# Kernel tuning notes

Hardware: AMD Instinct MI355X
Metric: run time of the kernel (lower is better)

## Reference

```python
import jax, jax.numpy as jnp
import numpy as np

S, P, H, E = 32, 32, 128, 64        # scenes, peds/scene, h_dim, embedding_dim
B1, B2 = 512, 1024                  # mlp_pre_pool hidden, bottleneck_dim
M1 = 1024                           # decoder mlp hidden
N = S * P
T = 12                              # seq_len (decode horizon)
BN_INV = 1.0 / np.sqrt(1.0 + 1e-5)  # eval-mode BatchNorm, running mean=0 var=1


def setup_inputs() -> dict:
    key = jax.random.key(0)
    ks = jax.random.split(key, 32)
    rn = lambda k, sh, s=0.05: jax.random.normal(k, sh, dtype=jnp.float32) * s
    inp = {
        'last_pos': rn(ks[0], (N, 2), 1.0),
        'last_pos_rel': rn(ks[1], (N, 2), 1.0),
        'h0': rn(ks[2], (N, H), 0.1),
        'c0': rn(ks[3], (N, H), 0.1),
        'seq_start_end': jnp.stack([jnp.arange(S) * P, (jnp.arange(S) + 1) * P], 1).astype(jnp.int32),
        # decoder spatial embedding Linear(2, E)
        'emb_W': rn(ks[4], (E, 2)), 'emb_b': rn(ks[5], (E,)),
        # LSTM (torch gate order i,f,g,o)
        'lstm_Wih': rn(ks[6], (4 * H, E)), 'lstm_Whh': rn(ks[7], (4 * H, H)),
        'lstm_bih': rn(ks[8], (4 * H,)), 'lstm_bhh': rn(ks[9], (4 * H,)),
        # hidden2pos Linear(H, 2)
        'pos_W': rn(ks[10], (2, H)), 'pos_b': rn(ks[11], (2,)),
        # pool_net spatial embedding Linear(2, E)
        'sp_W': rn(ks[12], (E, 2)), 'sp_b': rn(ks[13], (E,)),
        # mlp_pre_pool: Linear(E+H, 512)+BN+ReLU, Linear(512, 1024)+BN+ReLU
        'pp1_W': rn(ks[14], (B1, E + H)), 'pp1_b': rn(ks[15], (B1,)),
        'pp1_g': 1.0 + rn(ks[16], (B1,)), 'pp1_be': rn(ks[17], (B1,)),
        'pp2_W': rn(ks[18], (B2, B1)), 'pp2_b': rn(ks[19], (B2,)),
        'pp2_g': 1.0 + rn(ks[20], (B2,)), 'pp2_be': rn(ks[21], (B2,)),
        # decoder mlp: Linear(H+1024, 1024)+BN+ReLU, Linear(1024, H)+BN+ReLU
        'm1_W': rn(ks[22], (M1, H + B2)), 'm1_b': rn(ks[23], (M1,)),
        'm1_g': 1.0 + rn(ks[24], (M1,)), 'm1_be': rn(ks[25], (M1,)),
        'm2_W': rn(ks[26], (H, M1)), 'm2_b': rn(ks[27], (H,)),
        'm2_g': 1.0 + rn(ks[28], (H,)), 'm2_be': rn(ks[29], (H,)),
    }
    return inp


def _bn(x, g, b):
    return x * BN_INV * g + b


def reference(last_pos, last_pos_rel, h0, c0, seq_start_end,
              emb_W, emb_b, lstm_Wih, lstm_Whh, lstm_bih, lstm_bhh,
              pos_W, pos_b, sp_W, sp_b,
              pp1_W, pp1_b, pp1_g, pp1_be, pp2_W, pp2_b, pp2_g, pp2_be,
              m1_W, m1_b, m1_g, m1_be, m2_W, m2_b, m2_g, m2_be):
    # seq_start_end encodes uniform scenes of size P; pooling is done per scene.
    def step(carry, _):
        h, c, lp, din = carry  # h,c:[N,H]  lp:[N,2]  din:[N,E]
        gates = din @ lstm_Wih.T + lstm_bih + h @ lstm_Whh.T + lstm_bhh
        i, f, g_, o = jnp.split(gates, 4, axis=-1)
        c2 = jax.nn.sigmoid(f) * c + jax.nn.sigmoid(i) * jnp.tanh(g_)
        h2 = jax.nn.sigmoid(o) * jnp.tanh(c2)
        rel_pos = h2 @ pos_W.T + pos_b          # [N,2]
        curr = rel_pos + lp                     # [N,2]
        # ---- PoolHiddenNet: per-scene all-pairs gather -> MLP -> max ----
        ps = curr.reshape(S, P, 2)
        rel = ps[:, None, :, :] - ps[:, :, None, :]   # [s,i,j] = pos_j - pos_i
        rel = rel / jnp.maximum(jnp.linalg.norm(rel, axis=-1, keepdims=True), 1e-12)
        emb = rel @ sp_W.T + sp_b                      # [S,P,P,E]
        hj = jnp.broadcast_to(h2.reshape(S, 1, P, H), (S, P, P, H))
        x = jnp.concatenate([emb, hj], -1)             # [S,P,P,E+H]
        x = jax.nn.relu(_bn(x @ pp1_W.T + pp1_b, pp1_g, pp1_be))
        x = jax.nn.relu(_bn(x @ pp2_W.T + pp2_b, pp2_g, pp2_be))
        pool = x.max(axis=2).reshape(N, B2)            # max over neighbours j
        # ---- hidden refinement MLP ----
        dh = jnp.concatenate([h2, pool], 1)
        dh = jax.nn.relu(_bn(dh @ m1_W.T + m1_b, m1_g, m1_be))
        dh = jax.nn.relu(_bn(dh @ m2_W.T + m2_b, m2_g, m2_be))
        din2 = rel_pos @ emb_W.T + emb_b
        return (dh, c2, curr, din2), rel_pos

    din0 = last_pos_rel @ emb_W.T + emb_b
    _, preds = jax.lax.scan(step, (h0, c0, last_pos, din0), None, length=T)
    return preds  # [T, N, 2] predicted relative displacements
```

## Files before the change

### kernel.cpp

```cpp
#include <hip/hip_runtime.h>
#include <hip/hip_bf16.h>
#include <math.h>

#define DEVFN __device__ __forceinline__

constexpr float BN_INV = 0.99999500003749971f;

DEVFN float sigm(float x) { return 1.0f / (1.0f + expf(-x)); }

DEVFN unsigned short f2bf(float f) {
    __hip_bfloat16 b = __float2bfloat16(f);
    return *reinterpret_cast<unsigned short*>(&b);
}
DEVFN float bf2f(unsigned short u) {
    unsigned int x = ((unsigned int)u) << 16;
    return *reinterpret_cast<float*>(&x);
}
DEVFN void splitf(float v, unsigned short& h, unsigned short& l) {
    h = f2bf(v);
    l = f2bf(v - bf2f(h));
}
DEVFN unsigned int pack2(unsigned short a, unsigned short b) {
    return (unsigned int)a | ((unsigned int)b << 16);
}

typedef __attribute__((ext_vector_type(8))) short short8;
typedef __attribute__((ext_vector_type(4))) float f32x4;

#define ASYNC_COPY16(gsrc, ldst)                                                            \
    __builtin_amdgcn_global_load_lds((const __attribute__((address_space(1))) unsigned int*)(gsrc), \
                                     (__attribute__((address_space(3))) unsigned int*)(ldst), 16, 0, 0)


__global__ void pre_misc(
    const float* __restrict__ Wih, const float* __restrict__ Whh,
    const float* __restrict__ bih, const float* __restrict__ bhh,
    float* __restrict__ WgT, float* __restrict__ bg,
    const float* __restrict__ pp1W, const float* __restrict__ pp1g,
    float* __restrict__ Wh1T,
    const float* __restrict__ spW, const float* __restrict__ spb,
    const float* __restrict__ pp1b, const float* __restrict__ pp1be,
    float* __restrict__ Mp, float* __restrict__ c1,
    const float* __restrict__ lp, const float* __restrict__ lpr,
    const float* __restrict__ h0, const float* __restrict__ c0,
    const float* __restrict__ embW, const float* __restrict__ embb,
    float* __restrict__ h_st, float* __restrict__ c_st,
    float* __restrict__ curr, float* __restrict__ din) {
    int bid = blockIdx.x, t = threadIdx.x;
    if (bid < 384) {
        int idx = bid * 256 + t;
        int k = idx >> 9, tt = idx & 511;
        WgT[idx] = (k < 64) ? Wih[tt * 64 + k] : Whh[tt * 128 + (k - 64)];
        if (idx < 512) bg[idx] = bih[idx] + bhh[idx];
    } else if (bid < 640) {
        int idx = (bid - 384) * 256 + t;
        int h = idx >> 9, k = idx & 511;
        Wh1T[idx] = pp1W[k * 192 + 64 + h] * (BN_INV * pp1g[k]);
    } else if (bid < 642) {
        int k = (bid - 640) * 256 + t;
        float m0 = 0.f, m1 = 0.f, c0v = 0.f;
        for (int e = 0; e < 64; e++) {
            float w = pp1W[k * 192 + e];
            m0 += spW[e * 2] * w; m1 += spW[e * 2 + 1] * w; c0v += spb[e] * w;
        }
        float s = BN_INV * pp1g[k];
        Mp[k] = m0 * s; Mp[512 + k] = m1 * s;
        c1[k] = (c0v + pp1b[k]) * s + pp1be[k];
    } else {
        int idx = (bid - 642) * 256 + t;
        h_st[idx] = h0[idx];
        c_st[idx] = c0[idx];
        if (idx < 1024 * 2) curr[idx] = lp[idx];
        if (idx < 1024 * 64) {
            int n = idx >> 6, e = idx & 63;
            din[idx] = fmaf(lpr[n * 2], embW[e * 2], fmaf(lpr[n * 2 + 1], embW[e * 2 + 1], embb[e]));
        }
    }
}

__global__ void pre_w2bf(const float* __restrict__ W, const float* __restrict__ b,
                         const float* __restrict__ g, const float* __restrict__ be,
                         unsigned short* __restrict__ Wbf, float* __restrict__ cv, int swz) {
    int idx = blockIdx.x * blockDim.x + threadIdx.x;
    int ko = idx >> 9, k = idx & 511;
    float s = BN_INV * g[ko];
    int outk = swz ? ((k & ~63) | ((((k >> 3) & 7) ^ (ko & 7)) << 3) | (k & 7)) : k;
    Wbf[(ko << 9) + outk] = f2bf(W[idx] * s);
    if (idx < 1024) cv[idx] = b[idx] * s + be[idx];
}

__global__ void pre_w1split(const float* __restrict__ W, const float* __restrict__ b,
                            const float* __restrict__ g, const float* __restrict__ be,
                            unsigned short* __restrict__ Wh, unsigned short* __restrict__ Wl,
                            float* __restrict__ cv) {
    int idx = blockIdx.x * blockDim.x + threadIdx.x;
    int ko = idx / 1152;
    float s = BN_INV * g[ko];
    unsigned short h, l;
    splitf(W[idx] * s, h, l);
    Wh[idx] = h; Wl[idx] = l;
    if (idx < 1024) {
        float s2 = BN_INV * g[idx];
        cv[idx] = b[idx] * s2 + be[idx];
    }
}

__global__ void pre_w2split(const float* __restrict__ W, const float* __restrict__ b,
                            const float* __restrict__ g, const float* __restrict__ be,
                            unsigned short* __restrict__ Wh, unsigned short* __restrict__ Wl,
                            float* __restrict__ cv) {
    int idx = blockIdx.x * blockDim.x + threadIdx.x;
    int ko = idx >> 10;
    float s = BN_INV * g[ko];
    unsigned short h, l;
    splitf(W[idx] * s, h, l);
    Wh[idx] = h; Wl[idx] = l;
    if (idx < 128) {
        float s2 = BN_INV * g[idx];
        cv[idx] = b[idx] * s2 + be[idx];
    }
}


__global__ __launch_bounds__(512) void k_lstm(
    const float* __restrict__ WgT, const float* __restrict__ bg,
    float* __restrict__ h_st, float* __restrict__ c_st,
    float* __restrict__ din, float* __restrict__ curr,
    unsigned short* __restrict__ h2h, unsigned short* __restrict__ h2l,
    const float* __restrict__ posW, const float* __restrict__ posb,
    const float* __restrict__ embW, const float* __restrict__ embb,
    const float* __restrict__ Wh1T, const float* __restrict__ c1,
    float* __restrict__ Hp, int doHp,
    float* __restrict__ preds) {
    int n0 = blockIdx.x << 2;
    int t = threadIdx.x;
    __shared__ float xs[4][256];
    __shared__ float gates[4][512];
    __shared__ float h2s[4][128];
    __shared__ float rp[4][2];
#pragma unroll
    for (int u = 0; u < 2; u++) {
        int lin = t + (u << 9);
        int r = lin >> 8, k = lin & 255;
        float v = 0.f;
        if (k < 64) v = din[(n0 + r) * 64 + k];
        else if (k < 192) v = h_st[(n0 + r) * 128 + (k - 64)];
        xs[r][k] = v;
    }
    __syncthreads();
    float a0 = bg[t], a1 = a0, a2 = a0, a3 = a0;
#pragma unroll 4
    for (int k = 0; k < 192; k++) {
        float w = WgT[(k << 9) + t];
        a0 = fmaf(xs[0][k], w, a0);
        a1 = fmaf(xs[1][k], w, a1);
        a2 = fmaf(xs[2][k], w, a2);
        a3 = fmaf(xs[3][k], w, a3);
    }
    gates[0][t] = a0; gates[1][t] = a1; gates[2][t] = a2; gates[3][t] = a3;
    __syncthreads();
    {
        int r = t >> 7, hx = t & 127;
        float ig = sigm(gates[r][hx]);
        float fg = sigm(gates[r][128 + hx]);
        float gg = tanhf(gates[r][256 + hx]);
        float og = sigm(gates[r][384 + hx]);
        float c2 = fmaf(fg, c_st[(n0 + r) * 128 + hx], ig * gg);
        float h2 = og * tanhf(c2);
        c_st[(n0 + r) * 128 + hx] = c2;
        unsigned short sh, sl;
        splitf(h2, sh, sl);
        h2h[(n0 + r) * 128 + hx] = sh;
        h2l[(n0 + r) * 128 + hx] = sl;
        h2s[r][hx] = h2;
    }
    __syncthreads();
    int wv = t >> 6, l = t & 63;
    if (wv < 4) {
        float p0 = fmaf(h2s[wv][l], posW[l], h2s[wv][l + 64] * posW[l + 64]);
        float p1 = fmaf(h2s[wv][l], posW[128 + l], h2s[wv][l + 64] * posW[192 + l]);
#pragma unroll
        for (int off = 32; off > 0; off >>= 1) {
            p0 += __shfl_down(p0, off, 64);
            p1 += __shfl_down(p1, off, 64);
        }
        if (l == 0) { rp[wv][0] = p0 + posb[0]; rp[wv][1] = p1 + posb[1]; }
    }
    __syncthreads();
    if (t < 256) {
        int r = t >> 6, e = t & 63;
        float r0 = rp[r][0], r1 = rp[r][1];
        din[(n0 + r) * 64 + e] = fmaf(r0, embW[e * 2], fmaf(r1, embW[e * 2 + 1], embb[e]));
        if (e == 0) {
            preds[(n0 + r) * 2] = r0; preds[(n0 + r) * 2 + 1] = r1;
            curr[(n0 + r) * 2] += r0; curr[(n0 + r) * 2 + 1] += r1;
        }
    }
    if (doHp) {
        float cc = c1[t];
        float q0 = cc, q1 = cc, q2 = cc, q3 = cc;
#pragma unroll 4
        for (int h = 0; h < 128; h++) {
            float w = Wh1T[(h << 9) + t];
            q0 = fmaf(h2s[0][h], w, q0);
            q1 = fmaf(h2s[1][h], w, q1);
            q2 = fmaf(h2s[2][h], w, q2);
            q3 = fmaf(h2s[3][h], w, q3);
        }
        Hp[((n0 + 0) << 9) + t] = q0;
        Hp[((n0 + 1) << 9) + t] = q1;
        Hp[((n0 + 2) << 9) + t] = q2;
        Hp[((n0 + 3) << 9) + t] = q3;
    }
}

__global__ __launch_bounds__(256) void k_x1(
    const float* __restrict__ Hp, const float* __restrict__ Mp,
    const float* __restrict__ curr, unsigned short* __restrict__ x1g) {
    int bid = blockIdx.x;
    int c = bid & 7, q = bid >> 3;
    int i = q & 31, g = q >> 5;
    int s = (g << 3) + c;
    int si = (s << 5) + i;
    int t = threadIdx.x;
    __shared__ float rx[32], ry[32];
    __shared__ float m0s[512], m1s[512];
    for (int u = t; u < 512; u += 256) { m0s[u] = Mp[u]; m1s[u] = Mp[512 + u]; }
    if (t < 32) {
        int jg = (s << 5) + t;
        float dx = curr[jg * 2] - curr[si * 2];
        float dy = curr[jg * 2 + 1] - curr[si * 2 + 1];
        float den = fmaxf(sqrtf(dx * dx + dy * dy), 1e-12f);
        rx[t] = dx / den; ry[t] = dy / den;
    }
    __syncthreads();
    int j = t >> 3, c8 = t & 7;
    float rxv = rx[j], ryv = ry[j];
    const float* hp = Hp + (((s << 5) + j) << 9);
    unsigned short* op = x1g + ((size_t)((si << 5) + j) << 9);
    int swz = (c8 ^ (j & 7)) << 3;
#pragma unroll
    for (int kt = 0; kt < 512; kt += 64) {
        int k = kt + (c8 << 3);
        float4 ha = *(const float4*)(hp + k);
        float4 hb = *(const float4*)(hp + k + 4);
        uint4 o;
        o.x = pack2(f2bf(fmaxf(fmaf(rxv, m0s[k + 0], fmaf(ryv, m1s[k + 0], ha.x)), 0.f)),
                    f2bf(fmaxf(fmaf(rxv, m0s[k + 1], fmaf(ryv, m1s[k + 1], ha.y)), 0.f)));
        o.y = pack2(f2bf(fmaxf(fmaf(rxv, m0s[k + 2], fmaf(ryv, m1s[k + 2], ha.z)), 0.f)),
                    f2bf(fmaxf(fmaf(rxv, m0s[k + 3], fmaf(ryv, m1s[k + 3], ha.w)), 0.f)));
        o.z = pack2(f2bf(fmaxf(fmaf(rxv, m0s[k + 4], fmaf(ryv, m1s[k + 4], hb.x)), 0.f)),
                    f2bf(fmaxf(fmaf(rxv, m0s[k + 5], fmaf(ryv, m1s[k + 5], hb.y)), 0.f)));
        o.w = pack2(f2bf(fmaxf(fmaf(rxv, m0s[k + 6], fmaf(ryv, m1s[k + 6], hb.z)), 0.f)),
                    f2bf(fmaxf(fmaf(rxv, m0s[k + 7], fmaf(ryv, m1s[k + 7], hb.w)), 0.f)));
        *(uint4*)(op + kt + swz) = o;
    }
}

__global__ __launch_bounds__(1024, 4) void k_pool_g(
    const unsigned short* __restrict__ x1g, const unsigned short* __restrict__ W2bf,
    const float* __restrict__ c2v,
    unsigned short* __restrict__ poolh, unsigned short* __restrict__ pooll) {
    int bid = blockIdx.x;
    int c = bid & 7, q = bid >> 3;
    int inner = q & 15, g = q >> 4;
    int s = (g << 3) + c;
    int rb = inner >> 2;
    int koB = (inner & 3) << 8;
    int t = threadIdx.x;
    int lane = t & 63, wv = t >> 6;
    int quad = lane >> 4, l15 = lane & 15;
    int wr = wv >> 2, wc = wv & 3;
    int qrow = wr << 6, qcol = wc << 6;
    __shared__ unsigned short As[2][256 * 64];
    __shared__ unsigned short Bs[2][256 * 64];
    f32x4 acc[4][4];
#pragma unroll
    for (int a = 0; a < 4; a++)
#pragma unroll
        for (int b = 0; b < 4; b++) acc[a][b] = (f32x4){0.f, 0.f, 0.f, 0.f};

    int rlane = lane >> 3;
    int clane = (lane & 7) << 3;
    const unsigned short* gA = x1g + (size_t)((s << 10) + (rb << 8) + (wv << 4) + rlane) * 512 + clane;
    const unsigned short* gB = W2bf + (size_t)(koB + (wv << 4) + rlane) * 512 + clane;
    const unsigned short* pa0 = &As[0][((qrow + l15) << 6) + ((quad ^ (l15 & 7)) << 3)];
    const unsigned short* pb0 = &Bs[0][((qcol + l15) << 6) + ((quad ^ (l15 & 7)) << 3)];
    const unsigned short* pa1 = &As[0][((qrow + l15) << 6) + (((4 + quad) ^ (l15 & 7)) << 3)];
    const unsigned short* pb1 = &Bs[0][((qcol + l15) << 6) + (((4 + quad) ^ (l15 & 7)) << 3)];

#define POOL_STAGE(kt, buf)                                           \
    do {                                                              \
        unsigned short* lA = &As[buf][wv << 10];                      \
        unsigned short* lB = &Bs[buf][wv << 10];                      \
        ASYNC_COPY16(gA + (kt), lA);                                  \
        ASYNC_COPY16(gA + (kt) + 8 * 512, lA + (8 << 6));             \
        ASYNC_COPY16(gB + (kt), lB);                                  \
        ASYNC_COPY16(gB + (kt) + 8 * 512, lB + (8 << 6));             \
    } while (0)

    POOL_STAGE(0, 0);
    __syncthreads();
    for (int i = 0; i < 8; i++) {
        if (i < 7) POOL_STAGE((i + 1) << 6, (i + 1) & 1);
        int off = (i & 1) << 14;
        short8 aF[4], bF[4];
#pragma unroll
        for (int a = 0; a < 4; a++) aF[a] = *(const short8*)(pa0 + off + (a << 10));
#pragma unroll
        for (int b = 0; b < 4; b++) bF[b] = *(const short8*)(pb0 + off + (b << 10));
#pragma unroll
        for (int a = 0; a < 4; a++)
#pragma unroll
            for (int b = 0; b < 4; b++)
                acc[a][b] = __builtin_amdgcn_mfma_f32_16x16x32_bf16(aF[a], bF[b], acc[a][b], 0, 0, 0);
#pragma unroll
        for (int a = 0; a < 4; a++) aF[a] = *(const short8*)(pa1 + off + (a << 10));
#pragma unroll
        for (int b = 0; b < 4; b++) bF[b] = *(const short8*)(pb1 + off + (b << 10));
#pragma unroll
        for (int a = 0; a < 4; a++)
#pragma unroll
            for (int b = 0; b < 4; b++)
                acc[a][b] = __builtin_amdgcn_mfma_f32_16x16x32_bf16(aF[a], bF[b], acc[a][b], 0, 0, 0);
        __syncthreads();
    }
#undef POOL_STAGE

    float mx0[4], mx1[4];
#pragma unroll
    for (int b = 0; b < 4; b++) {
        float m = acc[0][b].x;
#pragma unroll
        for (int a = 0; a < 2; a++) {
            m = fmaxf(m, acc[a][b].x); m = fmaxf(m, acc[a][b].y);
            m = fmaxf(m, acc[a][b].z); m = fmaxf(m, acc[a][b].w);
        }
        m = fmaxf(m, __shfl_xor(m, 16));
        m = fmaxf(m, __shfl_xor(m, 32));
        mx0[b] = m;
        float n = acc[2][b].x;
#pragma unroll
        for (int a = 2; a < 4; a++) {
            n = fmaxf(n, acc[a][b].x); n = fmaxf(n, acc[a][b].y);
            n = fmaxf(n, acc[a][b].z); n = fmaxf(n, acc[a][b].w);
        }
        n = fmaxf(n, __shfl_xor(n, 16));
        n = fmaxf(n, __shfl_xor(n, 32));
        mx1[b] = n;
    }
    float v0 = (quad == 0) ? mx0[0] : (quad == 1) ? mx0[1] : (quad == 2) ? mx0[2] : mx0[3];
    float v1 = (quad == 0) ? mx1[0] : (quad == 1) ? mx1[1] : (quad == 2) ? mx1[2] : mx1[3];
    int col = koB + qcol + (quad << 4) + l15;
    int i0 = (rb << 3) + (wr << 1);
    int si0 = (s << 5) + i0;
    float bias = c2v[col];
    float w0 = fmaxf(v0 + bias, 0.f);
    float w1 = fmaxf(v1 + bias, 0.f);
    unsigned short h0, l0, h1, l1;
    splitf(w0, h0, l0); splitf(w1, h1, l1);
    poolh[si0 * 1024 + col] = h0; pooll[si0 * 1024 + col] = l0;
    poolh[(si0 + 1) * 1024 + col] = h1; pooll[(si0 + 1) * 1024 + col] = l1;
}

__global__ __launch_bounds__(256) void k_pool_mfma(
    const float* __restrict__ Hp, const float* __restrict__ Mp,
    const unsigned short* __restrict__ W2bf,
    const float* __restrict__ c2v, const float* __restrict__ curr,
    unsigned short* __restrict__ poolh, unsigned short* __restrict__ pooll) {
    int s = blockIdx.z;
    int rb = blockIdx.y;
    int koBase = blockIdx.x << 7;
    int t = threadIdx.x;
    int lane = t & 63, wv = t >> 6;
    int quad = lane >> 4, l15 = lane & 15;
    int qrow = (wv >> 1) << 6;
    int qcol = (wv & 1) << 6;

    __shared__ unsigned short As[128 * 40];
    __shared__ unsigned short Bs[128 * 40];
    __shared__ float rx[128], ry[128];

    if (t < 128) {
        int iL = t >> 5, j = t & 31;
        int ig = (s << 5) + (rb << 2) + iL;
        int jg = (s << 5) + j;
        float dx = curr[jg * 2] - curr[ig * 2];
        float dy = curr[jg * 2 + 1] - curr[ig * 2 + 1];
        float den = fmaxf(sqrtf(dx * dx + dy * dy), 1e-12f);
        rx[t] = dx / den; ry[t] = dy / den;
    }
    __syncthreads();

    f32x4 acc[4][4];
#pragma unroll
    for (int a = 0; a < 4; a++)
#pragma unroll
        for (int b = 0; b < 4; b++) acc[a][b] = (f32x4){0.f, 0.f, 0.f, 0.f};

    int r0 = t >> 3, c4 = (t & 7) << 2;
    int bn = t >> 1, bk = (t & 1) << 4;

    for (int kt = 0; kt < 512; kt += 32) {
#pragma unroll
        for (int p = 0; p < 4; p++) {
            int rr = r0 + (p << 5);
            int j = rr & 31;
            int kg = kt + c4;
            float4 hv = *(const float4*)(Hp + (((s << 5) + j) << 9) + kg);
            float4 m0 = *(const float4*)(Mp + kg);
            float4 m1 = *(const float4*)(Mp + 512 + kg);
            float rxv = rx[rr], ryv = ry[rr];
            float v0 = fmaxf(fmaf(rxv, m0.x, fmaf(ryv, m1.x, hv.x)), 0.f);
            float v1 = fmaxf(fmaf(rxv, m0.y, fmaf(ryv, m1.y, hv.y)), 0.f);
            float v2 = fmaxf(fmaf(rxv, m0.z, fmaf(ryv, m1.z, hv.z)), 0.f);
            float v3 = fmaxf(fmaf(rxv, m0.w, fmaf(ryv, m1.w, hv.w)), 0.f);
            unsigned int u0 = pack2(f2bf(v0), f2bf(v1));
            unsigned int u1 = pack2(f2bf(v2), f2bf(v3));
            *(uint2*)(&As[rr * 40 + c4]) = make_uint2(u0, u1);
        }
        {
            const unsigned short* src = W2bf + (((koBase + bn) << 9) + kt + bk);
            uint4 w0 = *(const uint4*)src;
            uint4 w1 = *(const uint4*)(src + 8);
            *(uint4*)(&Bs[bn * 40 + bk]) = w0;
            *(uint4*)(&Bs[bn * 40 + bk + 8]) = w1;
        }
        __syncthreads();
        short8 bF[4];
#pragma unroll
        for (int b = 0; b < 4; b++)
            bF[b] = *(const short8*)(&Bs[(qcol + (b << 4) + l15) * 40 + (quad << 3)]);
#pragma unroll
        for (int a = 0; a < 4; a++) {
            short8 aF = *(const short8*)(&As[(qrow + (a << 4) + l15) * 40 + (quad << 3)]);
#pragma unroll
            for (int b = 0; b < 4; b++)
                acc[a][b] = __builtin_amdgcn_mfma_f32_16x16x32_bf16(aF, bF[b], acc[a][b], 0, 0, 0);
        }
        __syncthreads();
    }

    float mx0[4], mx1[4];
#pragma unroll
    for (int b = 0; b < 4; b++) {
        float m = acc[0][b].x;
#pragma unroll
        for (int a = 0; a < 2; a++) {
            m = fmaxf(m, acc[a][b].x); m = fmaxf(m, acc[a][b].y);
            m = fmaxf(m, acc[a][b].z); m = fmaxf(m, acc[a][b].w);
        }
        m = fmaxf(m, __shfl_xor(m, 16));
        m = fmaxf(m, __shfl_xor(m, 32));
        mx0[b] = m;
        float n = acc[2][b].x;
#pragma unroll
        for (int a = 2; a < 4; a++) {
            n = fmaxf(n, acc[a][b].x); n = fmaxf(n, acc[a][b].y);
            n = fmaxf(n, acc[a][b].z); n = fmaxf(n, acc[a][b].w);
        }
        n = fmaxf(n, __shfl_xor(n, 16));
        n = fmaxf(n, __shfl_xor(n, 32));
        mx1[b] = n;
    }
    float v0 = (quad == 0) ? mx0[0] : (quad == 1) ? mx0[1] : (quad == 2) ? mx0[2] : mx0[3];
    float v1 = (quad == 0) ? mx1[0] : (quad == 1) ? mx1[1] : (quad == 2) ? mx1[2] : mx1[3];
    int col = koBase + qcol + (quad << 4) + l15;
    int i0 = (rb << 2) + ((wv >> 1) << 1);
    int si0 = (s << 5) + i0;
    float bias = c2v[col];
    float w0 = fmaxf(v0 + bias, 0.f);
    float w1 = fmaxf(v1 + bias, 0.f);
    unsigned short h0, l0, h1, l1;
    splitf(w0, h0, l0); splitf(w1, h1, l1);
    poolh[si0 * 1024 + col] = h0; pooll[si0 * 1024 + col] = l0;
    poolh[(si0 + 1) * 1024 + col] = h1; pooll[(si0 + 1) * 1024 + col] = l1;
}

__global__ __launch_bounds__(256) void k_m1_mfma(
    const unsigned short* __restrict__ h2h, const unsigned short* __restrict__ h2l,
    const unsigned short* __restrict__ poolh, const unsigned short* __restrict__ pooll,
    const unsigned short* __restrict__ M1h, const unsigned short* __restrict__ M1l,
    const float* __restrict__ cm1,
    unsigned short* __restrict__ dh1h, unsigned short* __restrict__ dh1l) {
    int rowBase = blockIdx.y << 6;
    int koBase = blockIdx.x << 6;
    int t = threadIdx.x;
    int lane = t & 63, wv = t >> 6;
    int quad = lane >> 4, l15 = lane & 15;
    int qrow = (wv >> 1) << 5, qcol = (wv & 1) << 5;
    __shared__ unsigned short Ah[64 * 72], Al[64 * 72], Bh[64 * 72], Bl[64 * 72];
    f32x4 acc[2][2];
#pragma unroll
    for (int a = 0; a < 2; a++)
#pragma unroll
        for (int b = 0; b < 2; b++) acc[a][b] = (f32x4){0.f, 0.f, 0.f, 0.f};

    int ar = t >> 2, ak = (t & 3) << 4;

    for (int kt = 0; kt < 1152; kt += 64) {
        {
            const unsigned short* sH;
            const unsigned short* sL;
            int off;
            if (kt < 128) {
                off = (rowBase + ar) * 128 + kt + ak;
                sH = h2h; sL = h2l;
            } else {
                off = (rowBase + ar) * 1024 + (kt - 128) + ak;
                sH = poolh; sL = pooll;
            }
            *(uint4*)&Ah[ar * 72 + ak] = *(const uint4*)(sH + off);
            *(uint4*)&Ah[ar * 72 + ak + 8] = *(const uint4*)(sH + off + 8);
            *(uint4*)&Al[ar * 72 + ak] = *(const uint4*)(sL + off);
            *(uint4*)&Al[ar * 72 + ak + 8] = *(const uint4*)(sL + off + 8);
        }
        {
            int boff = (koBase + ar) * 1152 + kt + ak;
            *(uint4*)&Bh[ar * 72 + ak] = *(const uint4*)(M1h + boff);
            *(uint4*)&Bh[ar * 72 + ak + 8] = *(const uint4*)(M1h + boff + 8);
            *(uint4*)&Bl[ar * 72 + ak] = *(const uint4*)(M1l + boff);
            *(uint4*)&Bl[ar * 72 + ak + 8] = *(const uint4*)(M1l + boff + 8);
        }
        __syncthreads();
#pragma unroll
        for (int kk2 = 0; kk2 < 2; kk2++) {
            int kc = ((kk2 << 2) | quad) << 3;
            short8 bH[2], bL[2];
#pragma unroll
            for (int b = 0; b < 2; b++) {
                int boff = (qcol + (b << 4) + l15) * 72 + kc;
                bH[b] = *(const short8*)(&Bh[boff]);
                bL[b] = *(const short8*)(&Bl[boff]);
            }
#pragma unroll
            for (int a = 0; a < 2; a++) {
                int aoff = (qrow + (a << 4) + l15) * 72 + kc;
                short8 aH = *(const short8*)(&Ah[aoff]);
                short8 aL = *(const short8*)(&Al[aoff]);
#pragma unroll
                for (int b = 0; b < 2; b++) {
                    acc[a][b] = __builtin_amdgcn_mfma_f32_16x16x32_bf16(aH, bH[b], acc[a][b], 0, 0, 0);
                    acc[a][b] = __builtin_amdgcn_mfma_f32_16x16x32_bf16(aH, bL[b], acc[a][b], 0, 0, 0);
                    acc[a][b] = __builtin_amdgcn_mfma_f32_16x16x32_bf16(aL, bH[b], acc[a][b], 0, 0, 0);
                }
            }
        }
        __syncthreads();
    }
#pragma unroll
    for (int b = 0; b < 2; b++) {
        int col = koBase + qcol + (b << 4) + l15;
        float bias = cm1[col];
#pragma unroll
        for (int a = 0; a < 2; a++) {
#pragma unroll
            for (int rg = 0; rg < 4; rg++) {
                int row = rowBase + qrow + (a << 4) + (quad << 2) + rg;
                float v = fmaxf(acc[a][b][rg] + bias, 0.f);
                unsigned short sh, sl;
                splitf(v, sh, sl);
                dh1h[row * 1024 + col] = sh;
                dh1l[row * 1024 + col] = sl;
            }
        }
    }
}

__global__ __launch_bounds__(256) void k_m2_mfma(
    const unsigned short* __restrict__ dh1h, const unsigned short* __restrict__ dh1l,
    const unsigned short* __restrict__ M2h, const unsigned short* __restrict__ M2l,
    const float* __restrict__ cm2, float* __restrict__ h_st) {
    int rowBase = blockIdx.x << 5;
    int t = threadIdx.x;
    int lane = t & 63, wv = t >> 6;
    int quad = lane >> 4, l15 = lane & 15;
    int qrow = (wv >> 1) << 4;
    int qcol = (wv & 1) << 6;
    __shared__ unsigned short Ah[32 * 40], Al[32 * 40], Bh[128 * 40], Bl[128 * 40];
    f32x4 acc[4];
#pragma unroll
    for (int b = 0; b < 4; b++) acc[b] = (f32x4){0.f, 0.f, 0.f, 0.f};

    int ar = t >> 3, ak = (t & 7) << 2;
    int br = t >> 1, bk = (t & 1) << 4;

    for (int kt = 0; kt < 1024; kt += 32) {
        {
            int off = (rowBase + ar) * 1024 + kt + ak;
            *(uint2*)&Ah[ar * 40 + ak] = *(const uint2*)(dh1h + off);
            *(uint2*)&Al[ar * 40 + ak] = *(const uint2*)(dh1l + off);
        }
        {
            int off = br * 1024 + kt + bk;
            *(uint4*)&Bh[br * 40 + bk] = *(const uint4*)(M2h + off);
            *(uint4*)&Bh[br * 40 + bk + 8] = *(const uint4*)(M2h + off + 8);
            *(uint4*)&Bl[br * 40 + bk] = *(const uint4*)(M2l + off);
            *(uint4*)&Bl[br * 40 + bk + 8] = *(const uint4*)(M2l + off + 8);
        }
        __syncthreads();
        {
            int aoff = (qrow + l15) * 40 + (quad << 3);
            short8 aH = *(const short8*)(&Ah[aoff]);
            short8 aL = *(const short8*)(&Al[aoff]);
#pragma unroll
            for (int b = 0; b < 4; b++) {
                int boff = (qcol + (b << 4) + l15) * 40 + (quad << 3);
                short8 bH = *(const short8*)(&Bh[boff]);
                short8 bL = *(const short8*)(&Bl[boff]);
                acc[b] = __builtin_amdgcn_mfma_f32_16x16x32_bf16(aH, bH, acc[b], 0, 0, 0);
                acc[b] = __builtin_amdgcn_mfma_f32_16x16x32_bf16(aH, bL, acc[b], 0, 0, 0);
                acc[b] = __builtin_amdgcn_mfma_f32_16x16x32_bf16(aL, bH, acc[b], 0, 0, 0);
            }
        }
        __syncthreads();
    }
#pragma unroll
    for (int b = 0; b < 4; b++) {
        int col = qcol + (b << 4) + l15;
        float bias = cm2[col];
#pragma unroll
        for (int rg = 0; rg < 4; rg++) {
            int row = rowBase + qrow + (quad << 2) + rg;
            h_st[row * 128 + col] = fmaxf(acc[b][rg] + bias, 0.f);
        }
    }
}


extern "C" void kernel_launch(void* const* d_in, const int* in_sizes, int n_in,
                              void* d_out, int out_size, void* d_ws, size_t ws_size,
                              hipStream_t stream) {
    const float* last_pos     = (const float*)d_in[0];
    const float* last_pos_rel = (const float*)d_in[1];
    const float* h0   = (const float*)d_in[2];
    const float* c0   = (const float*)d_in[3];
    const float* emb_W = (const float*)d_in[5];
    const float* emb_b = (const float*)d_in[6];
    const float* lstm_Wih = (const float*)d_in[7];
    const float* lstm_Whh = (const float*)d_in[8];
    const float* lstm_bih = (const float*)d_in[9];
    const float* lstm_bhh = (const float*)d_in[10];
    const float* pos_W = (const float*)d_in[11];
    const float* pos_b = (const float*)d_in[12];
    const float* sp_W  = (const float*)d_in[13];
    const float* sp_b  = (const float*)d_in[14];
    const float* pp1_W = (const float*)d_in[15];
    const float* pp1_b = (const float*)d_in[16];
    const float* pp1_g = (const float*)d_in[17];
    const float* pp1_be= (const float*)d_in[18];
    const float* pp2_W = (const float*)d_in[19];
    const float* pp2_b = (const float*)d_in[20];
    const float* pp2_g = (const float*)d_in[21];
    const float* pp2_be= (const float*)d_in[22];
    const float* m1_W  = (const float*)d_in[23];
    const float* m1_b  = (const float*)d_in[24];
    const float* m1_g  = (const float*)d_in[25];
    const float* m1_be = (const float*)d_in[26];
    const float* m2_W  = (const float*)d_in[27];
    const float* m2_b  = (const float*)d_in[28];
    const float* m2_g  = (const float*)d_in[29];
    const float* m2_be = (const float*)d_in[30];
    float* out = (float*)d_out;

    float* p = (float*)d_ws;
    float* WgT  = p; p += 192 * 512;
    float* bg   = p; p += 512;
    float* Wh1T = p; p += 128 * 512;
    float* Mp   = p; p += 2 * 512;
    float* c1   = p; p += 512;
    unsigned short* W2bf = (unsigned short*)p; p += 512 * 1024 / 2;
    float* c2v  = p; p += 1024;
    unsigned short* M1h = (unsigned short*)p; p += 1024 * 1152 / 2;
    unsigned short* M1l = (unsigned short*)p; p += 1024 * 1152 / 2;
    float* cm1  = p; p += 1024;
    unsigned short* M2h = (unsigned short*)p; p += 128 * 1024 / 2;
    unsigned short* M2l = (unsigned short*)p; p += 128 * 1024 / 2;
    float* cm2  = p; p += 128;
    float* h_st = p; p += 1024 * 128;
    float* c_st = p; p += 1024 * 128;
    unsigned short* h2h = (unsigned short*)p; p += 1024 * 128 / 2;
    unsigned short* h2l = (unsigned short*)p; p += 1024 * 128 / 2;
    float* curr = p; p += 1024 * 2;
    float* din  = p; p += 1024 * 64;
    float* Hp   = p; p += 1024 * 512;
    unsigned short* poolh = (unsigned short*)p; p += 1024 * 1024 / 2;
    unsigned short* pooll = (unsigned short*)p; p += 1024 * 1024 / 2;
    unsigned short* dh1h = (unsigned short*)p; p += 1024 * 1024 / 2;
    unsigned short* dh1l = (unsigned short*)p; p += 1024 * 1024 / 2;
    unsigned short* x1g = (unsigned short*)p;
    size_t need = (size_t)((char*)(x1g + (size_t)32768 * 512) - (char*)d_ws);
    int big = (ws_size >= need) ? 1 : 0;

    pre_misc<<<1154, 256, 0, stream>>>(lstm_Wih, lstm_Whh, lstm_bih, lstm_bhh, WgT, bg,
                                       pp1_W, pp1_g, Wh1T,
                                       sp_W, sp_b, pp1_b, pp1_be, Mp, c1,
                                       last_pos, last_pos_rel, h0, c0, emb_W, emb_b,
                                       h_st, c_st, curr, din);
    pre_w2bf<<<2048, 256, 0, stream>>>(pp2_W, pp2_b, pp2_g, pp2_be, W2bf, c2v, big);
    pre_w1split<<<4608, 256, 0, stream>>>(m1_W, m1_b, m1_g, m1_be, M1h, M1l, cm1);
    pre_w2split<<<512, 256, 0, stream>>>(m2_W, m2_b, m2_g, m2_be, M2h, M2l, cm2);

    for (int t = 0; t < 12; t++) {
        k_lstm<<<256, 512, 0, stream>>>(WgT, bg, h_st, c_st, din, curr, h2h, h2l,
                                        pos_W, pos_b, emb_W, emb_b,
                                        Wh1T, c1, Hp, (t < 11) ? 1 : 0, out + t * 2048);
        if (t == 11) break;
        if (big) {
            k_x1<<<1024, 256, 0, stream>>>(Hp, Mp, curr, x1g);
            k_pool_g<<<512, 1024, 0, stream>>>(x1g, W2bf, c2v, poolh, pooll);
        } else {
            k_pool_mfma<<<dim3(8, 8, 32), 256, 0, stream>>>(Hp, Mp, W2bf, c2v, curr,
                                                            poolh, pooll);
        }
        k_m1_mfma<<<dim3(16, 16), 256, 0, stream>>>(h2h, h2l, poolh, pooll,
                                                    M1h, M1l, cm1, dh1h, dh1l);
        k_m2_mfma<<<32, 256, 0, stream>>>(dh1h, dh1l, M2h, M2l, cm2, h_st);
    }
}
```

Measured before the change: 1.387 ms.

## Interleave bf16 hi/lo split pairs into packed words and merge weight prep kernels

The separate hi and lo bf16 arrays for h2, pool, dh1 and the m1/m2 weights are replaced by one 32-bit word per element holding both halves. Consumers load them with wide vector loads and unzip into separate LDS tiles. This turns two scattered 16-bit stores per element into one 32-bit store and halves the number of load streams in the GEMM kernels, at the cost of extra bit manipulation. The three weight-prep kernels are merged into one launch, and k_m1 blocks are remapped to a 1D grid with a swizzled row/column assignment.

```diff
diff --git a/kernel.cpp b/kernel.cpp
--- a/kernel.cpp
+++ b/kernel.cpp
@@ -23,9 +23,29 @@
 DEVFN unsigned int pack2(unsigned short a, unsigned short b) {
     return (unsigned int)a | ((unsigned int)b << 16);
 }
+DEVFN unsigned int packsplit(float v) {
+    unsigned short h, l;
+    splitf(v, h, l);
+    return pack2(h, l);
+}
 
 typedef __attribute__((ext_vector_type(8))) short short8;
 typedef __attribute__((ext_vector_type(4))) float f32x4;
+
+DEVFN void unzip16(unsigned short* dh, unsigned short* dl,
+                   uint4 a0, uint4 a1, uint4 a2, uint4 a3) {
+    uint4 h0, h1, l0, l1;
+    h0.x = (a0.x & 0xffffu) | (a0.y << 16); l0.x = (a0.x >> 16) | (a0.y & 0xffff0000u);
+    h0.y = (a0.z & 0xffffu) | (a0.w << 16); l0.y = (a0.z >> 16) | (a0.w & 0xffff0000u);
+    h0.z = (a1.x & 0xffffu) | (a1.y << 16); l0.z = (a1.x >> 16) | (a1.y & 0xffff0000u);
+    h0.w = (a1.z & 0xffffu) | (a1.w << 16); l0.w = (a1.z >> 16) | (a1.w & 0xffff0000u);
+    h1.x = (a2.x & 0xffffu) | (a2.y << 16); l1.x = (a2.x >> 16) | (a2.y & 0xffff0000u);
+    h1.y = (a2.z & 0xffffu) | (a2.w << 16); l1.y = (a2.z >> 16) | (a2.w & 0xffff0000u);
+    h1.z = (a3.x & 0xffffu) | (a3.y << 16); l1.z = (a3.x >> 16) | (a3.y & 0xffff0000u);
+    h1.w = (a3.z & 0xffffu) | (a3.w << 16); l1.w = (a3.z >> 16) | (a3.w & 0xffff0000u);
+    *(uint4*)dh = h0; *(uint4*)(dh + 8) = h1;
+    *(uint4*)dl = l0; *(uint4*)(dl + 8) = l1;
+}
 
 #define ASYNC_COPY16(gsrc, ldst)                                                            \
     __builtin_amdgcn_global_load_lds((const __attribute__((address_space(1))) unsigned int*)(gsrc), \
@@ -78,46 +98,42 @@
     }
 }
 
-__global__ void pre_w2bf(const float* __restrict__ W, const float* __restrict__ b,
-                         const float* __restrict__ g, const float* __restrict__ be,
-                         unsigned short* __restrict__ Wbf, float* __restrict__ cv, int swz) {
-    int idx = blockIdx.x * blockDim.x + threadIdx.x;
-    int ko = idx >> 9, k = idx & 511;
-    float s = BN_INV * g[ko];
-    int outk = swz ? ((k & ~63) | ((((k >> 3) & 7) ^ (ko & 7)) << 3) | (k & 7)) : k;
-    Wbf[(ko << 9) + outk] = f2bf(W[idx] * s);
-    if (idx < 1024) cv[idx] = b[idx] * s + be[idx];
-}
-
-__global__ void pre_w1split(const float* __restrict__ W, const float* __restrict__ b,
-                            const float* __restrict__ g, const float* __restrict__ be,
-                            unsigned short* __restrict__ Wh, unsigned short* __restrict__ Wl,
-                            float* __restrict__ cv) {
-    int idx = blockIdx.x * blockDim.x + threadIdx.x;
-    int ko = idx / 1152;
-    float s = BN_INV * g[ko];
-    unsigned short h, l;
-    splitf(W[idx] * s, h, l);
-    Wh[idx] = h; Wl[idx] = l;
-    if (idx < 1024) {
-        float s2 = BN_INV * g[idx];
-        cv[idx] = b[idx] * s2 + be[idx];
-    }
-}
-
-__global__ void pre_w2split(const float* __restrict__ W, const float* __restrict__ b,
-                            const float* __restrict__ g, const float* __restrict__ be,
-                            unsigned short* __restrict__ Wh, unsigned short* __restrict__ Wl,
-                            float* __restrict__ cv) {
-    int idx = blockIdx.x * blockDim.x + threadIdx.x;
-    int ko = idx >> 10;
-    float s = BN_INV * g[ko];
-    unsigned short h, l;
-    splitf(W[idx] * s, h, l);
-    Wh[idx] = h; Wl[idx] = l;
-    if (idx < 128) {
-        float s2 = BN_INV * g[idx];
-        cv[idx] = b[idx] * s2 + be[idx];
+__global__ void pre_w(
+    const float* __restrict__ pp2W, const float* __restrict__ pp2b,
+    const float* __restrict__ pp2g, const float* __restrict__ pp2be,
+    unsigned short* __restrict__ W2bf, float* __restrict__ c2v, int swz,
+    const float* __restrict__ m1W, const float* __restrict__ m1b,
+    const float* __restrict__ m1g, const float* __restrict__ m1be,
+    unsigned int* __restrict__ M1p, float* __restrict__ cm1,
+    const float* __restrict__ m2W, const float* __restrict__ m2b,
+    const float* __restrict__ m2g, const float* __restrict__ m2be,
+    unsigned int* __restrict__ M2p, float* __restrict__ cm2) {
+    int bid = blockIdx.x, t = threadIdx.x;
+    if (bid < 2048) {
+        int idx = bid * 256 + t;
+        int ko = idx >> 9, k = idx & 511;
+        float s = BN_INV * pp2g[ko];
+        int outk = swz ? ((k & ~63) | ((((k >> 3) & 7) ^ (ko & 7)) << 3) | (k & 7)) : k;
+        W2bf[(ko << 9) + outk] = f2bf(pp2W[idx] * s);
+        if (idx < 1024) c2v[idx] = pp2b[idx] * s + pp2be[idx];
+    } else if (bid < 6656) {
+        int idx = (bid - 2048) * 256 + t;
+        int ko = idx / 1152;
+        float s = BN_INV * m1g[ko];
+        M1p[idx] = packsplit(m1W[idx] * s);
+        if (idx < 1024) {
+            float s2 = BN_INV * m1g[idx];
+            cm1[idx] = m1b[idx] * s2 + m1be[idx];
+        }
+    } else {
+        int idx = (bid - 6656) * 256 + t;
+        int ko = idx >> 10;
+        float s = BN_INV * m2g[ko];
+        M2p[idx] = packsplit(m2W[idx] * s);
+        if (idx < 128) {
+            float s2 = BN_INV * m2g[idx];
+            cm2[idx] = m2b[idx] * s2 + m2be[idx];
+        }
     }
 }
 
@@ -126,7 +142,7 @@
     const float* __restrict__ WgT, const float* __restrict__ bg,
     float* __restrict__ h_st, float* __restrict__ c_st,
     float* __restrict__ din, float* __restrict__ curr,
-    unsigned short* __restrict__ h2h, unsigned short* __restrict__ h2l,
+    unsigned int* __restrict__ h2p,
     const float* __restrict__ posW, const float* __restrict__ posb,
     const float* __restrict__ embW, const float* __restrict__ embb,
     const float* __restrict__ Wh1T, const float* __restrict__ c1,
@@ -168,10 +184,7 @@
         float c2 = fmaf(fg, c_st[(n0 + r) * 128 + hx], ig * gg);
         float h2 = og * tanhf(c2);
         c_st[(n0 + r) * 128 + hx] = c2;
-        unsigned short sh, sl;
-        splitf(h2, sh, sl);
-        h2h[(n0 + r) * 128 + hx] = sh;
-        h2l[(n0 + r) * 128 + hx] = sl;
+        h2p[(n0 + r) * 128 + hx] = packsplit(h2);
         h2s[r][hx] = h2;
     }
     __syncthreads();
@@ -260,7 +273,7 @@
 __global__ __launch_bounds__(1024, 4) void k_pool_g(
     const unsigned short* __restrict__ x1g, const unsigned short* __restrict__ W2bf,
     const float* __restrict__ c2v,
-    unsigned short* __restrict__ poolh, unsigned short* __restrict__ pooll) {
+    unsigned int* __restrict__ poolp) {
     int bid = blockIdx.x;
     int c = bid & 7, q = bid >> 3;
     int inner = q & 15, g = q >> 4;
@@ -355,19 +368,15 @@
     int i0 = (rb << 3) + (wr << 1);
     int si0 = (s << 5) + i0;
     float bias = c2v[col];
-    float w0 = fmaxf(v0 + bias, 0.f);
-    float w1 = fmaxf(v1 + bias, 0.f);
-    unsigned short h0, l0, h1, l1;
-    splitf(w0, h0, l0); splitf(w1, h1, l1);
-    poolh[si0 * 1024 + col] = h0; pooll[si0 * 1024 + col] = l0;
-    poolh[(si0 + 1) * 1024 + col] = h1; pooll[(si0 + 1) * 1024 + col] = l1;
+    poolp[si0 * 1024 + col] = packsplit(fmaxf(v0 + bias, 0.f));
+    poolp[(si0 + 1) * 1024 + col] = packsplit(fmaxf(v1 + bias, 0.f));
 }
 
 __global__ __launch_bounds__(256) void k_pool_mfma(
     const float* __restrict__ Hp, const float* __restrict__ Mp,
     const unsigned short* __restrict__ W2bf,
     const float* __restrict__ c2v, const float* __restrict__ curr,
-    unsigned short* __restrict__ poolh, unsigned short* __restrict__ pooll) {
+    unsigned int* __restrict__ poolp) {
     int s = blockIdx.z;
     int rb = blockIdx.y;
     int koBase = blockIdx.x << 7;
@@ -469,22 +478,20 @@
     int i0 = (rb << 2) + ((wv >> 1) << 1);
     int si0 = (s << 5) + i0;
     float bias = c2v[col];
-    float w0 = fmaxf(v0 + bias, 0.f);
-    float w1 = fmaxf(v1 + bias, 0.f);
-    unsigned short h0, l0, h1, l1;
-    splitf(w0, h0, l0); splitf(w1, h1, l1);
-    poolh[si0 * 1024 + col] = h0; pooll[si0 * 1024 + col] = l0;
-    poolh[(si0 + 1) * 1024 + col] = h1; pooll[(si0 + 1) * 1024 + col] = l1;
+    poolp[si0 * 1024 + col] = packsplit(fmaxf(v0 + bias, 0.f));
+    poolp[(si0 + 1) * 1024 + col] = packsplit(fmaxf(v1 + bias, 0.f));
 }
 
 __global__ __launch_bounds__(256) void k_m1_mfma(
-    const unsigned short* __restrict__ h2h, const unsigned short* __restrict__ h2l,
-    const unsigned short* __restrict__ poolh, const unsigned short* __restrict__ pooll,
-    const unsigned short* __restrict__ M1h, const unsigned short* __restrict__ M1l,
-    const float* __restrict__ cm1,
-    unsigned short* __restrict__ dh1h, unsigned short* __restrict__ dh1l) {
-    int rowBase = blockIdx.y << 6;
-    int koBase = blockIdx.x << 6;
+    const unsigned int* __restrict__ h2p, const unsigned int* __restrict__ poolp,
+    const unsigned int* __restrict__ M1p, const float* __restrict__ cm1,
+    unsigned int* __restrict__ dh1p) {
+    int bid = blockIdx.x;
+    int c = bid & 7, q = bid >> 3;
+    int kg = (c << 1) | (q >> 4);
+    int rowg = q & 15;
+    int rowBase = rowg << 6;
+    int koBase = kg << 6;
     int t = threadIdx.x;
     int lane = t & 63, wv = t >> 6;
     int quad = lane >> 4, l15 = lane & 15;
@@ -500,27 +507,20 @@
 
     for (int kt = 0; kt < 1152; kt += 64) {
         {
-            const unsigned short* sH;
-            const unsigned short* sL;
-            int off;
-            if (kt < 128) {
-                off = (rowBase + ar) * 128 + kt + ak;
-                sH = h2h; sL = h2l;
-            } else {
-                off = (rowBase + ar) * 1024 + (kt - 128) + ak;
-                sH = poolh; sL = pooll;
-            }
-            *(uint4*)&Ah[ar * 72 + ak] = *(const uint4*)(sH + off);
-            *(uint4*)&Ah[ar * 72 + ak + 8] = *(const uint4*)(sH + off + 8);
-            *(uint4*)&Al[ar * 72 + ak] = *(const uint4*)(sL + off);
-            *(uint4*)&Al[ar * 72 + ak + 8] = *(const uint4*)(sL + off + 8);
-        }
-        {
-            int boff = (koBase + ar) * 1152 + kt + ak;
-            *(uint4*)&Bh[ar * 72 + ak] = *(const uint4*)(M1h + boff);
-            *(uint4*)&Bh[ar * 72 + ak + 8] = *(const uint4*)(M1h + boff + 8);
-            *(uint4*)&Bl[ar * 72 + ak] = *(const uint4*)(M1l + boff);
-            *(uint4*)&Bl[ar * 72 + ak + 8] = *(const uint4*)(M1l + boff + 8);
+            const unsigned int* srcA = (kt < 128)
+                ? h2p + (rowBase + ar) * 128 + kt + ak
+                : poolp + (rowBase + ar) * 1024 + (kt - 128) + ak;
+            uint4 a0 = ((const uint4*)srcA)[0];
+            uint4 a1 = ((const uint4*)srcA)[1];
+            uint4 a2 = ((const uint4*)srcA)[2];
+            uint4 a3 = ((const uint4*)srcA)[3];
+            const unsigned int* srcB = M1p + (koBase + ar) * 1152 + kt + ak;
+            uint4 b0 = ((const uint4*)srcB)[0];
+            uint4 b1 = ((const uint4*)srcB)[1];
+            uint4 b2 = ((const uint4*)srcB)[2];
+            uint4 b3 = ((const uint4*)srcB)[3];
+            unzip16(&Ah[ar * 72 + ak], &Al[ar * 72 + ak], a0, a1, a2, a3);
+            unzip16(&Bh[ar * 72 + ak], &Bl[ar * 72 + ak], b0, b1, b2, b3);
         }
         __syncthreads();
 #pragma unroll
@@ -557,19 +557,14 @@
 #pragma unroll
             for (int rg = 0; rg < 4; rg++) {
                 int row = rowBase + qrow + (a << 4) + (quad << 2) + rg;
-                float v = fmaxf(acc[a][b][rg] + bias, 0.f);
-                unsigned short sh, sl;
-                splitf(v, sh, sl);
-                dh1h[row * 1024 + col] = sh;
-                dh1l[row * 1024 + col] = sl;
+                dh1p[row * 1024 + col] = packsplit(fmaxf(acc[a][b][rg] + bias, 0.f));
             }
         }
     }
 }
 
 __global__ __launch_bounds__(256) void k_m2_mfma(
-    const unsigned short* __restrict__ dh1h, const unsigned short* __restrict__ dh1l,
-    const unsigned short* __restrict__ M2h, const unsigned short* __restrict__ M2l,
+    const unsigned int* __restrict__ dh1p, const unsigned int* __restrict__ M2p,
     const float* __restrict__ cm2, float* __restrict__ h_st) {
     int rowBase = blockIdx.x << 5;
     int t = threadIdx.x;
@@ -587,16 +582,21 @@
 
     for (int kt = 0; kt < 1024; kt += 32) {
         {
-            int off = (rowBase + ar) * 1024 + kt + ak;
-            *(uint2*)&Ah[ar * 40 + ak] = *(const uint2*)(dh1h + off);
-            *(uint2*)&Al[ar * 40 + ak] = *(const uint2*)(dh1l + off);
+            uint4 av = *(const uint4*)(dh1p + (rowBase + ar) * 1024 + kt + ak);
+            uint2 hi = make_uint2((av.x & 0xffffu) | (av.y << 16),
+                                  (av.z & 0xffffu) | (av.w << 16));
+            uint2 lo = make_uint2((av.x >> 16) | (av.y & 0xffff0000u),
+                                  (av.z >> 16) | (av.w & 0xffff0000u));
+            *(uint2*)&Ah[ar * 40 + ak] = hi;
+            *(uint2*)&Al[ar * 40 + ak] = lo;
         }
         {
-            int off = br * 1024 + kt + bk;
-            *(uint4*)&Bh[br * 40 + bk] = *(const uint4*)(M2h + off);
-            *(uint4*)&Bh[br * 40 + bk + 8] = *(const uint4*)(M2h + off + 8);
-            *(uint4*)&Bl[br * 40 + bk] = *(const uint4*)(M2l + off);
-            *(uint4*)&Bl[br * 40 + bk + 8] = *(const uint4*)(M2l + off + 8);
+            const unsigned int* srcB = M2p + br * 1024 + kt + bk;
+            uint4 b0 = ((const uint4*)srcB)[0];
+            uint4 b1 = ((const uint4*)srcB)[1];
+            uint4 b2 = ((const uint4*)srcB)[2];
+            uint4 b3 = ((const uint4*)srcB)[3];
+            unzip16(&Bh[br * 40 + bk], &Bl[br * 40 + bk], b0, b1, b2, b3);
         }
         __syncthreads();
         {
@@ -671,23 +671,18 @@
     float* c1   = p; p += 512;
     unsigned short* W2bf = (unsigned short*)p; p += 512 * 1024 / 2;
     float* c2v  = p; p += 1024;
-    unsigned short* M1h = (unsigned short*)p; p += 1024 * 1152 / 2;
-    unsigned short* M1l = (unsigned short*)p; p += 1024 * 1152 / 2;
+    unsigned int* M1p = (unsigned int*)p; p += 1024 * 1152;
     float* cm1  = p; p += 1024;
-    unsigned short* M2h = (unsigned short*)p; p += 128 * 1024 / 2;
-    unsigned short* M2l = (unsigned short*)p; p += 128 * 1024 / 2;
+    unsigned int* M2p = (unsigned int*)p; p += 128 * 1024;
     float* cm2  = p; p += 128;
     float* h_st = p; p += 1024 * 128;
     float* c_st = p; p += 1024 * 128;
-    unsigned short* h2h = (unsigned short*)p; p += 1024 * 128 / 2;
-    unsigned short* h2l = (unsigned short*)p; p += 1024 * 128 / 2;
+    unsigned int* h2p = (unsigned int*)p; p += 1024 * 128;
     float* curr = p; p += 1024 * 2;
     float* din  = p; p += 1024 * 64;
     float* Hp   = p; p += 1024 * 512;
-    unsigned short* poolh = (unsigned short*)p; p += 1024 * 1024 / 2;
-    unsigned short* pooll = (unsigned short*)p; p += 1024 * 1024 / 2;
-    unsigned short* dh1h = (unsigned short*)p; p += 1024 * 1024 / 2;
-    unsigned short* dh1l = (unsigned short*)p; p += 1024 * 1024 / 2;
+    unsigned int* poolp = (unsigned int*)p; p += 1024 * 1024;
+    unsigned int* dh1p = (unsigned int*)p; p += 1024 * 1024;
     unsigned short* x1g = (unsigned short*)p;
     size_t need = (size_t)((char*)(x1g + (size_t)32768 * 512) - (char*)d_ws);
     int big = (ws_size >= need) ? 1 : 0;
@@ -697,24 +692,22 @@
                                        sp_W, sp_b, pp1_b, pp1_be, Mp, c1,
                                        last_pos, last_pos_rel, h0, c0, emb_W, emb_b,
                                        h_st, c_st, curr, din);
-    pre_w2bf<<<2048, 256, 0, stream>>>(pp2_W, pp2_b, pp2_g, pp2_be, W2bf, c2v, big);
-    pre_w1split<<<4608, 256, 0, stream>>>(m1_W, m1_b, m1_g, m1_be, M1h, M1l, cm1);
-    pre_w2split<<<512, 256, 0, stream>>>(m2_W, m2_b, m2_g, m2_be, M2h, M2l, cm2);
+    pre_w<<<7168, 256, 0, stream>>>(pp2_W, pp2_b, pp2_g, pp2_be, W2bf, c2v, big,
+                                    m1_W, m1_b, m1_g, m1_be, M1p, cm1,
+                                    m2_W, m2_b, m2_g, m2_be, M2p, cm2);
 
     for (int t = 0; t < 12; t++) {
-        k_lstm<<<256, 512, 0, stream>>>(WgT, bg, h_st, c_st, din, curr, h2h, h2l,
+        k_lstm<<<256, 512, 0, stream>>>(WgT, bg, h_st, c_st, din, curr, h2p,
                                         pos_W, pos_b, emb_W, emb_b,
                                         Wh1T, c1, Hp, (t < 11) ? 1 : 0, out + t * 2048);
         if (t == 11) break;
         if (big) {
             k_x1<<<1024, 256, 0, stream>>>(Hp, Mp, curr, x1g);
-            k_pool_g<<<512, 1024, 0, stream>>>(x1g, W2bf, c2v, poolh, pooll);
+            k_pool_g<<<512, 1024, 0, stream>>>(x1g, W2bf, c2v, poolp);
         } else {
-            k_pool_mfma<<<dim3(8, 8, 32), 256, 0, stream>>>(Hp, Mp, W2bf, c2v, curr,
-                                                            poolh, pooll);
-        }
-        k_m1_mfma<<<dim3(16, 16), 256, 0, stream>>>(h2h, h2l, poolh, pooll,
-                                                    M1h, M1l, cm1, dh1h, dh1l);
-        k_m2_mfma<<<32, 256, 0, stream>>>(dh1h, dh1l, M2h, M2l, cm2, h_st);
-    }
-}
+            k_pool_mfma<<<dim3(8, 8, 32), 256, 0, stream>>>(Hp, Mp, W2bf, c2v, curr, poolp);
+        }
+        k_m1_mfma<<<256, 256, 0, stream>>>(h2p, poolp, M1p, cm1, dh1p);
+        k_m2_mfma<<<32, 256, 0, stream>>>(dh1p, M2p, cm2, h_st);
+    }
+}
```

New measurement: 1.484 ms. +7.0%, slower.
